# Kernel tuning notes

Hardware: AMD Instinct MI355X
Metric: run time of the kernel (lower is better)

The kernel has to match this reference:

```python
import jax, jax.numpy as jnp
import numpy as np
from jax import lax

EPS = 1e-12  # F.normalize default eps
NUM_HEADS = 3
TEMP = 1.0

def setup_inputs() -> dict:
    key = jax.random.key(0)
    ks = jax.random.split(key, 7)
    b, c, h, w = 4, 96, 256, 256
    s = 0.02
    return {
        'x': jax.random.normal(ks[0], (b, c, h, w), jnp.float32),
        'qkv_w': jax.random.normal(ks[1], (3 * c, c), jnp.float32) * s,
        'qkv_b': jax.random.normal(ks[2], (3 * c,), jnp.float32) * s,
        'dw_w': jax.random.normal(ks[3], (3 * c, 1, 3, 3), jnp.float32) * s,
        'dw_b': jax.random.normal(ks[4], (3 * c,), jnp.float32) * s,
        'proj_w': jax.random.normal(ks[5], (c, c), jnp.float32) * s,
        'proj_b': jax.random.normal(ks[6], (c,), jnp.float32) * s,
    }

def _l2norm(t):
    # F.normalize over last dim: t / max(||t||, eps)
    n = jnp.sqrt(jnp.sum(t * t, axis=-1, keepdims=True))
    return t / jnp.maximum(n, EPS)

def reference(x, qkv_w, qkv_b, dw_w, dw_b, proj_w, proj_b):
    b, c, h, w = x.shape
    head = NUM_HEADS
    # 1x1 conv (pointwise) -> [b, 3c, h, w]
    qkv = jnp.einsum('oc,bchw->bohw', qkv_w, x) + qkv_b[None, :, None, None]
    # 3x3 depthwise conv, padding=1
    qkv = lax.conv_general_dilated(
        qkv, dw_w, window_strides=(1, 1), padding='SAME',
        feature_group_count=3 * c,
        dimension_numbers=('NCHW', 'OIHW', 'NCHW')) + dw_b[None, :, None, None]
    q, k, v = jnp.split(qkv, 3, axis=1)
    # b (head hc) h w -> b head hc (h w)
    def to_heads(t):
        return t.reshape(b, head, c // head, h * w)
    q, k, v = to_heads(q), to_heads(k), to_heads(v)
    q = _l2norm(q)
    k = _l2norm(k)
    # channel-wise attention scores: [b, head, hc, hc]
    attn = jnp.einsum('bhcn,bhdn->bhcd', q, k) * TEMP
    attn = jax.nn.softmax(attn, axis=-1)
    out = jnp.einsum('bhcd,bhdn->bhcn', attn, v)  # [b, head, hc, hw]
    out = out.reshape(b, c, h, w)
    out = jnp.einsum('oc,bchw->bohw', proj_w, out) + proj_b[None, :, None, None]
    return (out, attn)
```

## Files before the change

kernel.cpp:

```cpp
#include <hip/hip_runtime.h>
#include <hip/hip_bf16.h>

#define B_  4
#define C_  96
#define H_  256
#define W_  256
#define N_  (H_*W_)
#define C3_ 288
#define HEAD_ 3
#define HC_ 32
#define EPS_ 1e-12f
#define XP_ 104
#define SPLITS_ 128

typedef __attribute__((ext_vector_type(8))) short short8;
typedef __attribute__((ext_vector_type(4))) float f32x4;

__device__ __forceinline__ unsigned short f2bf(float f) {
  unsigned u = __float_as_uint(f);
  u += 0x7fffu + ((u >> 16) & 1u);
  return (unsigned short)(u >> 16);
}
__device__ __forceinline__ float bf2f(unsigned short h) {
  return __uint_as_float((unsigned)h << 16);
}
__device__ __forceinline__ float bf_lo(unsigned u) { return __uint_as_float(u << 16); }
__device__ __forceinline__ float bf_hi(unsigned u) { return __uint_as_float(u & 0xffff0000u); }
__device__ __forceinline__ unsigned pack_bf(float a, float b) {
  return (unsigned)f2bf(a) | ((unsigned)f2bf(b) << 16);
}
__device__ __forceinline__ unsigned cvt_pk(float lo, float hi) {
  unsigned r;
  asm("v_cvt_pk_bf16_f32 %0, %1, %2" : "=v"(r) : "v"(lo), "v"(hi));
  return r;
}

__global__ __launch_bounds__(512) void k1_mfma(
    const float* __restrict__ x, const float* __restrict__ wsrc,
    const float* __restrict__ bias, unsigned short* __restrict__ out) {
  __shared__ unsigned short Wl[C3_ * XP_];
  __shared__ float Bl[C3_];
  const int tid = threadIdx.x;
  const int b = blockIdx.y;
  for (int i = tid; i < (C3_ * C_) / 2; i += 512) {
    const int o = i / 48, c2 = i % 48;
    const float2 f = *reinterpret_cast<const float2*>(wsrc + o * 96 + c2 * 2);
    *reinterpret_cast<unsigned*>(&Wl[o * XP_ + c2 * 2]) = cvt_pk(f.x, f.y);
  }
  for (int i = tid; i < C3_; i += 512) Bl[i] = bias[i];
  __syncthreads();
  const int lane = tid & 63;
  const int wv = tid >> 6;
  const int l15 = lane & 15, quad = lane >> 4;
  const int pixbase = blockIdx.x * 128 + wv * 16;
  const float* xcol = x + (size_t)b * C_ * N_ + pixbase + l15;
  union { short8 s; unsigned u[4]; } ax[3];
#pragma unroll
  for (int kc = 0; kc < 3; ++kc) {
#pragma unroll
    for (int j = 0; j < 4; ++j) {
      const float f0 = xcol[(size_t)(kc * 32 + quad * 8 + 2 * j) * N_];
      const float f1 = xcol[(size_t)(kc * 32 + quad * 8 + 2 * j + 1) * N_];
      ax[kc].u[j] = cvt_pk(f0, f1);
    }
  }
  f32x4 acc[18];
#pragma unroll
  for (int m = 0; m < 18; ++m) acc[m] = (f32x4){0.f, 0.f, 0.f, 0.f};
#pragma unroll
  for (int m = 0; m < 18; ++m) {
#pragma unroll
    for (int kc = 0; kc < 3; ++kc) {
      const short8 wfr = *reinterpret_cast<const short8*>(
          &Wl[(m * 16 + l15) * XP_ + kc * 32 + quad * 8]);
      acc[m] = __builtin_amdgcn_mfma_f32_16x16x32_bf16(ax[kc].s, wfr, acc[m], 0, 0, 0);
    }
  }
  unsigned short* ob = out + (size_t)b * C3_ * N_ + pixbase + quad * 4;
#pragma unroll
  for (int m = 0; m < 18; ++m) {
    const float bv = Bl[m * 16 + l15];
    uint2 st;
    st.x = cvt_pk(acc[m][0] + bv, acc[m][1] + bv);
    st.y = cvt_pk(acc[m][2] + bv, acc[m][3] + bv);
    *reinterpret_cast<uint2*>(ob + (size_t)(m * 16 + l15) * N_) = st;
  }
}

__global__ __launch_bounds__(256) void k_dw_reg(
    unsigned short* a, const float* __restrict__ w9,
    const float* __restrict__ bias, float* __restrict__ inv) {
  const int bc = blockIdx.x;
  const int ch = bc % C3_;
  unsigned short* p = a + (size_t)bc * N_;
  const int tid = threadIdx.x;
  const int tr = tid >> 5;
  const int tc = tid & 31;
  const int x0 = tc * 8;
  const int y0 = tr * 32;
  float wv[9];
#pragma unroll
  for (int i = 0; i < 9; ++i) wv[i] = w9[ch * 9 + i];
  const float bv = bias[ch];

  auto load_row = [&](int y, float* d) {
    if ((unsigned)y >= 256u) {
#pragma unroll
      for (int j = 0; j < 10; ++j) d[j] = 0.f;
      return;
    }
    const unsigned short* rp = p + (size_t)y * W_;
    const uint4 u = *reinterpret_cast<const uint4*>(rp + x0);
    d[1] = bf_lo(u.x); d[2] = bf_hi(u.x); d[3] = bf_lo(u.y); d[4] = bf_hi(u.y);
    d[5] = bf_lo(u.z); d[6] = bf_hi(u.z); d[7] = bf_lo(u.w); d[8] = bf_hi(u.w);
    d[0] = (tc > 0) ? bf2f(rp[x0 - 1]) : 0.f;
    d[9] = (tc < 31) ? bf2f(rp[x0 + 8]) : 0.f;
  };

  float rm[10], rc[10], rn[10], rb[10];
  load_row(y0 - 1, rm);
  load_row(y0, rc);
  load_row(y0 + 1, rn);
  load_row(y0 + 32, rb);
  __syncthreads();

  float ss = 0.f;
  for (int y = y0; y < y0 + 32; ++y) {
    float o[8];
#pragma unroll
    for (int j = 0; j < 8; ++j) {
      o[j] = bv + wv[0] * rm[j] + wv[1] * rm[j + 1] + wv[2] * rm[j + 2]
                + wv[3] * rc[j] + wv[4] * rc[j + 1] + wv[5] * rc[j + 2]
                + wv[6] * rn[j] + wv[7] * rn[j + 1] + wv[8] * rn[j + 2];
      ss += o[j] * o[j];
    }
    uint4 st;
    st.x = pack_bf(o[0], o[1]); st.y = pack_bf(o[2], o[3]);
    st.z = pack_bf(o[4], o[5]); st.w = pack_bf(o[6], o[7]);
    *reinterpret_cast<uint4*>(p + (size_t)y * W_ + x0) = st;
#pragma unroll
    for (int j = 0; j < 10; ++j) { rm[j] = rc[j]; rc[j] = rn[j]; }
    const int ny = y + 2;
    if (ny <= y0 + 31) {
      load_row(ny, rn);
    } else if (ny == y0 + 32) {
#pragma unroll
      for (int j = 0; j < 10; ++j) rn[j] = rb[j];
    }
  }
#pragma unroll
  for (int off = 32; off > 0; off >>= 1) ss += __shfl_down(ss, off, 64);
  __shared__ float red[4];
  if ((tid & 63) == 0) red[tid >> 6] = ss;
  __syncthreads();
  if (tid == 0 && ch < 192) {
    const float t = red[0] + red[1] + red[2] + red[3];
    const int b = bc / C3_;
    inv[b * 192 + ch] = 1.0f / fmaxf(sqrtf(t), EPS_);
  }
}

__global__ __launch_bounds__(256) void k_attn_mfma(
    const unsigned short* __restrict__ dw, float* __restrict__ part) {
  const int tid = threadIdx.x;
  const int lane = tid & 63;
  const int wv = tid >> 6;
  const int i0 = (wv >> 1) * 16, j0 = (wv & 1) * 16;
  const int h = blockIdx.y, b = blockIdx.z;
  const int n0 = blockIdx.x * (N_ / SPLITS_);
  const int l15 = lane & 15, quad = lane >> 4;
  const unsigned short* qrow =
      dw + ((size_t)(b * C3_ + h * HC_ + i0 + l15)) * N_ + n0 + quad * 8;
  const unsigned short* krow =
      dw + ((size_t)(b * C3_ + C_ + h * HC_ + j0 + l15)) * N_ + n0 + quad * 8;
  f32x4 acc = (f32x4){0.f, 0.f, 0.f, 0.f};
#pragma unroll 8
  for (int s = 0; s < N_ / SPLITS_; s += 32) {
    const short8 af = *reinterpret_cast<const short8*>(qrow + s);
    const short8 bf = *reinterpret_cast<const short8*>(krow + s);
    acc = __builtin_amdgcn_mfma_f32_16x16x32_bf16(af, bf, acc, 0, 0, 0);
  }
  float* pp = part + (size_t)blockIdx.x * (B_ * HEAD_ * 1024)
                   + ((size_t)(b * HEAD_ + h)) * 1024;
#pragma unroll
  for (int r = 0; r < 4; ++r)
    pp[(i0 + quad * 4 + r) * 32 + j0 + l15] = acc[r];
}

__global__ __launch_bounds__(256) void k_softmax(
    const float* __restrict__ part, const float* __restrict__ inv,
    float* __restrict__ attn_out) {
  __shared__ float red[2][4][32];
  const int tid = threadIdx.x;
  {
    const int r2 = tid >> 7;
    const int loc = tid & 127;
    const int sg = loc >> 5;
    const int j = loc & 31;
    const int R = blockIdx.x * 2 + r2;
    float v = 0.f;
#pragma unroll 8
    for (int s = sg; s < SPLITS_; s += 4)
      v += part[(size_t)s * (B_ * HEAD_ * 1024) + R * 32 + j];
    red[r2][sg][j] = v;
  }
  __syncthreads();
  if (tid < 64) {
    const int r2 = tid >> 5, j = tid & 31;
    const int R = blockIdx.x * 2 + r2;
    const int b = R / 96, rem = R % 96;
    const int h = rem / 32, i = rem % 32;
    float v = red[r2][0][j] + red[r2][1][j] + red[r2][2][j] + red[r2][3][j];
    v *= inv[b * 192 + h * 32 + i] * inv[b * 192 + 96 + h * 32 + j];
    float m = v;
#pragma unroll
    for (int off = 16; off > 0; off >>= 1) m = fmaxf(m, __shfl_xor(m, off, 32));
    const float e = __expf(v - m);
    float s = e;
#pragma unroll
    for (int off = 16; off > 0; off >>= 1) s += __shfl_xor(s, off, 32);
    attn_out[R * 32 + j] = e / s;
  }
}

__global__ __launch_bounds__(256) void k_M(
    const float* __restrict__ attn, const float* __restrict__ proj_w,
    unsigned short* __restrict__ Mbf) {
  const int b = blockIdx.x, h = blockIdx.y;
  const int tid = threadIdx.x;
  __shared__ float As[1024];
  __shared__ float Pw[C_ * 32];
  for (int l = tid; l < 1024; l += 256)
    As[l] = attn[((size_t)b * HEAD_ + h) * 1024 + l];
  for (int l = tid; l < C_ * 32; l += 256)
    Pw[l] = proj_w[(l >> 5) * C_ + h * 32 + (l & 31)];
  __syncthreads();
  for (int e = tid; e < C_ * 32; e += 256) {
    const int o = e >> 5, j = e & 31;
    float s = 0.f;
#pragma unroll
    for (int i = 0; i < 32; ++i) s += Pw[o * 32 + i] * As[i * 32 + j];
    Mbf[(size_t)b * C_ * C_ + o * C_ + h * 32 + j] = f2bf(s);
  }
}

__global__ __launch_bounds__(256) void k7_mfma(
    const unsigned short* __restrict__ A ,
    const unsigned short* __restrict__ Mbf,
    const float* __restrict__ bias, float* __restrict__ out) {
  const int tid = threadIdx.x;
  const int b = blockIdx.y;
  const int lane = tid & 63;
  const int wv = tid >> 6;
  const int l15 = lane & 15, quad = lane >> 4;
  const int pixbase = blockIdx.x * 64 + wv * 16;
  const unsigned short* vcol = A + ((size_t)(b * C3_ + 2 * C_)) * N_ + pixbase + l15;
  const unsigned short* Mb = Mbf + (size_t)b * C_ * C_;
  short8 afr[3];
#pragma unroll
  for (int kc = 0; kc < 3; ++kc) {
#pragma unroll
    for (int u = 0; u < 8; ++u)
      afr[kc][u] = (short)vcol[(size_t)(kc * 32 + quad * 8 + u) * N_];
  }
  f32x4 acc[6];
#pragma unroll
  for (int m = 0; m < 6; ++m) acc[m] = (f32x4){0.f, 0.f, 0.f, 0.f};
#pragma unroll
  for (int m = 0; m < 6; ++m) {
#pragma unroll
    for (int kc = 0; kc < 3; ++kc) {
      const short8 mfr = *reinterpret_cast<const short8*>(
          Mb + (m * 16 + l15) * C_ + kc * 32 + quad * 8);
      acc[m] = __builtin_amdgcn_mfma_f32_16x16x32_bf16(afr[kc], mfr, acc[m], 0, 0, 0);
    }
  }
  float* ob = out + (size_t)b * C_ * N_ + pixbase + quad * 4;
#pragma unroll
  for (int m = 0; m < 6; ++m) {
    const float bv = bias[m * 16 + l15];
    f32x4 st;
#pragma unroll
    for (int r = 0; r < 4; ++r) st[r] = acc[m][r] + bv;
    *reinterpret_cast<f32x4*>(ob + (size_t)(m * 16 + l15) * N_) = st;
  }
}

extern "C" void kernel_launch(void* const* d_in, const int* in_sizes, int n_in,
                              void* d_out, int out_size, void* d_ws, size_t ws_size,
                              hipStream_t stream) {
  const float* x      = (const float*)d_in[0];
  const float* qkv_w  = (const float*)d_in[1];
  const float* qkv_b  = (const float*)d_in[2];
  const float* dw_w   = (const float*)d_in[3];
  const float* dw_b   = (const float*)d_in[4];
  const float* proj_w = (const float*)d_in[5];
  const float* proj_b = (const float*)d_in[6];

  float* out      = (float*)d_out;
  float* attn_out = out + (size_t)B_ * C_ * N_;

  unsigned short* A = (unsigned short*)d_ws;
  float* inv   = (float*)(A + (size_t)B_ * C3_ * N_);
  float* part  = inv + 768;
  unsigned short* Mbf = (unsigned short*)(part + SPLITS_ * B_ * HEAD_ * 1024);

  k1_mfma<<<dim3(N_ / 128, B_), 512, 0, stream>>>(x, qkv_w, qkv_b, A);
  k_dw_reg<<<B_ * C3_, 256, 0, stream>>>(A, dw_w, dw_b, inv);
  k_attn_mfma<<<dim3(SPLITS_, HEAD_, B_), 256, 0, stream>>>(A, part);
  k_softmax<<<192, 256, 0, stream>>>(part, inv, attn_out);
  k_M<<<dim3(B_, HEAD_), 256, 0, stream>>>(attn_out, proj_w, Mbf);
  k7_mfma<<<dim3(N_ / 64, B_), 256, 0, stream>>>(A, Mbf, proj_b, out);
}
```

Before: 374.7 us.

## Split qkv pointwise conv across output-channel groups and swap MFMA operand roles

The 1x1 qkv conv kernel now launches three blocks per pixel tile, each computing 96 of the 288 output channels. This cuts accumulator registers and LDS per block so occupancy and parallelism can rise. MFMA operands are swapped so weights are the A operand and pixels the B operand, giving lane-per-pixel output with scalar 16-bit stores instead of 64-bit stores. The cost is reading x three times and narrower, less coalesced-per-instruction stores.

After: 358.6 us. 4.3% less time.

```diff
diff --git a/kernel.cpp b/kernel.cpp
--- a/kernel.cpp
+++ b/kernel.cpp
@@ -38,52 +38,48 @@
 __global__ __launch_bounds__(512) void k1_mfma(
     const float* __restrict__ x, const float* __restrict__ wsrc,
     const float* __restrict__ bias, unsigned short* __restrict__ out) {
-  __shared__ unsigned short Wl[C3_ * XP_];
-  __shared__ float Bl[C3_];
-  const int tid = threadIdx.x;
-  const int b = blockIdx.y;
-  for (int i = tid; i < (C3_ * C_) / 2; i += 512) {
-    const int o = i / 48, c2 = i % 48;
-    const float2 f = *reinterpret_cast<const float2*>(wsrc + o * 96 + c2 * 2);
-    *reinterpret_cast<unsigned*>(&Wl[o * XP_ + c2 * 2]) = cvt_pk(f.x, f.y);
-  }
-  for (int i = tid; i < C3_; i += 512) Bl[i] = bias[i];
+  __shared__ unsigned short Wl[96 * XP_];
+  __shared__ float Bl[96];
+  const int tid = threadIdx.x;
+  const int och0 = blockIdx.y * 96;
+  const int b = blockIdx.z;
+  for (int i = tid; i < 96 * C_; i += 512) {
+    const int r = i / 96, c = i % 96;
+    Wl[r * XP_ + c] = f2bf(wsrc[(size_t)(och0 + r) * C_ + c]);
+  }
+  if (tid < 96) Bl[tid] = bias[och0 + tid];
   __syncthreads();
   const int lane = tid & 63;
   const int wv = tid >> 6;
   const int l15 = lane & 15, quad = lane >> 4;
-  const int pixbase = blockIdx.x * 128 + wv * 16;
-  const float* xcol = x + (size_t)b * C_ * N_ + pixbase + l15;
-  union { short8 s; unsigned u[4]; } ax[3];
+  const int gpix = blockIdx.x * 128 + wv * 16 + l15;
+  const float* xcol = x + (size_t)b * C_ * N_ + gpix;
+  f32x4 acc[6];
+#pragma unroll
+  for (int m = 0; m < 6; ++m) acc[m] = (f32x4){0.f, 0.f, 0.f, 0.f};
 #pragma unroll
   for (int kc = 0; kc < 3; ++kc) {
-#pragma unroll
-    for (int j = 0; j < 4; ++j) {
-      const float f0 = xcol[(size_t)(kc * 32 + quad * 8 + 2 * j) * N_];
-      const float f1 = xcol[(size_t)(kc * 32 + quad * 8 + 2 * j + 1) * N_];
-      ax[kc].u[j] = cvt_pk(f0, f1);
-    }
-  }
-  f32x4 acc[18];
-#pragma unroll
-  for (int m = 0; m < 18; ++m) acc[m] = (f32x4){0.f, 0.f, 0.f, 0.f};
-#pragma unroll
-  for (int m = 0; m < 18; ++m) {
-#pragma unroll
-    for (int kc = 0; kc < 3; ++kc) {
-      const short8 wfr = *reinterpret_cast<const short8*>(
+    short8 bfr;
+#pragma unroll
+    for (int u = 0; u < 8; ++u)
+      bfr[u] = (short)f2bf(xcol[(size_t)(kc * 32 + quad * 8 + u) * N_]);
+#pragma unroll
+    for (int m = 0; m < 6; ++m) {
+      const short8 afr = *reinterpret_cast<const short8*>(
           &Wl[(m * 16 + l15) * XP_ + kc * 32 + quad * 8]);
-      acc[m] = __builtin_amdgcn_mfma_f32_16x16x32_bf16(ax[kc].s, wfr, acc[m], 0, 0, 0);
-    }
-  }
-  unsigned short* ob = out + (size_t)b * C3_ * N_ + pixbase + quad * 4;
-#pragma unroll
-  for (int m = 0; m < 18; ++m) {
-    const float bv = Bl[m * 16 + l15];
-    uint2 st;
-    st.x = cvt_pk(acc[m][0] + bv, acc[m][1] + bv);
-    st.y = cvt_pk(acc[m][2] + bv, acc[m][3] + bv);
-    *reinterpret_cast<uint2*>(ob + (size_t)(m * 16 + l15) * N_) = st;
+      acc[m] = __builtin_amdgcn_mfma_f32_16x16x32_bf16(afr, bfr, acc[m], 0, 0, 0);
+    }
+  }
+  unsigned short* ob = out + ((size_t)b * C3_ + och0) * N_ + gpix;
+#pragma unroll
+  for (int m = 0; m < 6; ++m) {
+    const int chb = m * 16 + quad * 4;
+    const unsigned pk0 = cvt_pk(acc[m][0] + Bl[chb], acc[m][1] + Bl[chb + 1]);
+    const unsigned pk1 = cvt_pk(acc[m][2] + Bl[chb + 2], acc[m][3] + Bl[chb + 3]);
+    ob[(size_t)chb * N_]       = (unsigned short)(pk0 & 0xffffu);
+    ob[(size_t)(chb + 1) * N_] = (unsigned short)(pk0 >> 16);
+    ob[(size_t)(chb + 2) * N_] = (unsigned short)(pk1 & 0xffffu);
+    ob[(size_t)(chb + 3) * N_] = (unsigned short)(pk1 >> 16);
   }
 }
 
@@ -305,7 +301,7 @@
   float* part  = inv + 768;
   unsigned short* Mbf = (unsigned short*)(part + SPLITS_ * B_ * HEAD_ * 1024);
 
-  k1_mfma<<<dim3(N_ / 128, B_), 512, 0, stream>>>(x, qkv_w, qkv_b, A);
+  k1_mfma<<<dim3(N_ / 128, 3, B_), 512, 0, stream>>>(x, qkv_w, qkv_b, A);
   k_dw_reg<<<B_ * C3_, 256, 0, stream>>>(A, dw_w, dw_b, inv);
   k_attn_mfma<<<dim3(SPLITS_, HEAD_, B_), 256, 0, stream>>>(A, part);
   k_softmax<<<192, 256, 0, stream>>>(part, inv, attn_out);
```

## Make qkv pointwise kernel persistent and swap MFMA operand roles

Applied to the files above, without the earlier changes.

The 1x1 qkv convolution kernel now launches 512 blocks that loop over four pixel tiles each. The bf16 weight staging into LDS is paid once per block instead of once per tile. The MFMA operands are swapped so weights are the A operand and pixels the B operand, and per-channel bias is indexed accordingly. Output stores become scalar 16-bit writes per channel instead of packed 64-bit writes across pixels, which may reduce store coalescing efficiency.

Result: slower. 408.1 us (+8.9%).

```diff
diff --git a/kernel.cpp b/kernel.cpp
--- a/kernel.cpp
+++ b/kernel.cpp
@@ -41,49 +41,53 @@
   __shared__ unsigned short Wl[C3_ * XP_];
   __shared__ float Bl[C3_];
   const int tid = threadIdx.x;
-  const int b = blockIdx.y;
   for (int i = tid; i < (C3_ * C_) / 2; i += 512) {
-    const int o = i / 48, c2 = i % 48;
-    const float2 f = *reinterpret_cast<const float2*>(wsrc + o * 96 + c2 * 2);
-    *reinterpret_cast<unsigned*>(&Wl[o * XP_ + c2 * 2]) = cvt_pk(f.x, f.y);
+    const int o = i / 48, c2 = (i % 48) * 2;
+    const float2 f = *reinterpret_cast<const float2*>(wsrc + o * 96 + c2);
+    *reinterpret_cast<unsigned*>(&Wl[o * XP_ + c2]) = cvt_pk(f.x, f.y);
   }
   for (int i = tid; i < C3_; i += 512) Bl[i] = bias[i];
   __syncthreads();
   const int lane = tid & 63;
   const int wv = tid >> 6;
   const int l15 = lane & 15, quad = lane >> 4;
-  const int pixbase = blockIdx.x * 128 + wv * 16;
-  const float* xcol = x + (size_t)b * C_ * N_ + pixbase + l15;
-  union { short8 s; unsigned u[4]; } ax[3];
-#pragma unroll
-  for (int kc = 0; kc < 3; ++kc) {
-#pragma unroll
-    for (int j = 0; j < 4; ++j) {
-      const float f0 = xcol[(size_t)(kc * 32 + quad * 8 + 2 * j) * N_];
-      const float f1 = xcol[(size_t)(kc * 32 + quad * 8 + 2 * j + 1) * N_];
-      ax[kc].u[j] = cvt_pk(f0, f1);
-    }
-  }
-  f32x4 acc[18];
-#pragma unroll
-  for (int m = 0; m < 18; ++m) acc[m] = (f32x4){0.f, 0.f, 0.f, 0.f};
-#pragma unroll
-  for (int m = 0; m < 18; ++m) {
+  for (int t = blockIdx.x; t < 2048; t += 512) {
+    const int b = t >> 9, tile = t & 511;
+    const int gpix = tile * 128 + wv * 16 + l15;
+    const float* xcol = x + (size_t)b * C_ * N_ + gpix;
+    union { short8 s; unsigned u[4]; } bx[3];
 #pragma unroll
     for (int kc = 0; kc < 3; ++kc) {
-      const short8 wfr = *reinterpret_cast<const short8*>(
-          &Wl[(m * 16 + l15) * XP_ + kc * 32 + quad * 8]);
-      acc[m] = __builtin_amdgcn_mfma_f32_16x16x32_bf16(ax[kc].s, wfr, acc[m], 0, 0, 0);
-    }
-  }
-  unsigned short* ob = out + (size_t)b * C3_ * N_ + pixbase + quad * 4;
-#pragma unroll
-  for (int m = 0; m < 18; ++m) {
-    const float bv = Bl[m * 16 + l15];
-    uint2 st;
-    st.x = cvt_pk(acc[m][0] + bv, acc[m][1] + bv);
-    st.y = cvt_pk(acc[m][2] + bv, acc[m][3] + bv);
-    *reinterpret_cast<uint2*>(ob + (size_t)(m * 16 + l15) * N_) = st;
+#pragma unroll
+      for (int j = 0; j < 4; ++j) {
+        const float f0 = xcol[(size_t)(kc * 32 + quad * 8 + 2 * j) * N_];
+        const float f1 = xcol[(size_t)(kc * 32 + quad * 8 + 2 * j + 1) * N_];
+        bx[kc].u[j] = cvt_pk(f0, f1);
+      }
+    }
+    f32x4 acc[18];
+#pragma unroll
+    for (int m = 0; m < 18; ++m) acc[m] = (f32x4){0.f, 0.f, 0.f, 0.f};
+#pragma unroll
+    for (int m = 0; m < 18; ++m) {
+#pragma unroll
+      for (int kc = 0; kc < 3; ++kc) {
+        const short8 afr = *reinterpret_cast<const short8*>(
+            &Wl[(m * 16 + l15) * XP_ + kc * 32 + quad * 8]);
+        acc[m] = __builtin_amdgcn_mfma_f32_16x16x32_bf16(afr, bx[kc].s, acc[m], 0, 0, 0);
+      }
+    }
+    unsigned short* ob = out + (size_t)b * C3_ * N_ + gpix;
+#pragma unroll
+    for (int m = 0; m < 18; ++m) {
+      const int chb = m * 16 + quad * 4;
+      const unsigned pk0 = cvt_pk(acc[m][0] + Bl[chb], acc[m][1] + Bl[chb + 1]);
+      const unsigned pk1 = cvt_pk(acc[m][2] + Bl[chb + 2], acc[m][3] + Bl[chb + 3]);
+      ob[(size_t)chb * N_]       = (unsigned short)(pk0 & 0xffffu);
+      ob[(size_t)(chb + 1) * N_] = (unsigned short)(pk0 >> 16);
+      ob[(size_t)(chb + 2) * N_] = (unsigned short)(pk1 & 0xffffu);
+      ob[(size_t)(chb + 3) * N_] = (unsigned short)(pk1 >> 16);
+    }
   }
 }
 
@@ -303,9 +307,9 @@
   unsigned short* A = (unsigned short*)d_ws;
   float* inv   = (float*)(A + (size_t)B_ * C3_ * N_);
   float* part  = inv + 768;
-  unsigned short* Mbf = (unsigned short*)(part + SPLITS_ * B_ * HEAD_ * 1024);
-
-  k1_mfma<<<dim3(N_ / 128, B_), 512, 0, stream>>>(x, qkv_w, qkv_b, A);
+  unsigned short* Mbf = (unsigned short*)(part + (size_t)SPLITS_ * B_ * HEAD_ * 1024);
+
+  k1_mfma<<<512, 512, 0, stream>>>(x, qkv_w, qkv_b, A);
   k_dw_reg<<<B_ * C3_, 256, 0, stream>>>(A, dw_w, dw_b, inv);
   k_attn_mfma<<<dim3(SPLITS_, HEAD_, B_), 256, 0, stream>>>(A, part);
   k_softmax<<<192, 256, 0, stream>>>(part, inv, attn_out);
```
